# Performance work log

Measured on AMD Instinct MI355X. Metric: run time of the kernel, lower is better.

The kernel has to match this reference:

```python
import jax, jax.numpy as jnp
import numpy as np

B, S, HID = 2, 4096, 1024
H, D = 16, 64

def rotate_half(x):
    x1, x2 = jnp.split(x, 2, axis=-1)
    return jnp.concatenate([-x2, x1], axis=-1)

def setup_inputs() -> dict:
    key = jax.random.key(0)
    ks = jax.random.split(key, 8)
    hidden_states = jax.random.normal(ks[0], (B, S, HID), dtype=jnp.float32)
    pos = jnp.arange(S, dtype=jnp.float32)[:, None]
    inv_freq = 1.0 / (10000.0 ** (jnp.arange(0, D, 2, dtype=jnp.float32) / D))
    freqs = pos * inv_freq[None, :]
    emb = jnp.concatenate([freqs, freqs], axis=-1)  # [S, D]
    cos = jnp.cos(emb)
    sin = jnp.sin(emb)
    W_rkv = jax.random.normal(ks[1], (3 * H * D, HID), dtype=jnp.float32) * 0.02
    W_o = jax.random.normal(ks[2], (HID, H * D), dtype=jnp.float32) * 0.02
    # match torch init: uniform(-8,-5), uniform(-1,1), uniform(0.2,0.8)
    time_decay = jax.random.uniform(ks[3], (H, D), minval=-8.0, maxval=-5.0, dtype=jnp.float32)
    time_first = jax.random.uniform(ks[4], (H, D), minval=-1.0, maxval=1.0, dtype=jnp.float32)
    time_mix = jax.random.uniform(ks[5], (1, 1, HID), minval=0.2, maxval=0.8, dtype=jnp.float32)
    return {"hidden_states": hidden_states, "cos": cos, "sin": sin,
            "W_rkv": W_rkv, "W_o": W_o, "time_decay": time_decay,
            "time_first": time_first, "time_mix": time_mix}

def reference(hidden_states, cos, sin, W_rkv, W_o, time_decay, time_first, time_mix):
    b, s, hid = hidden_states.shape
    # token-shift time mixing
    xx = jnp.concatenate([jnp.zeros_like(hidden_states[:, :1]), hidden_states[:, :-1]], axis=1)
    mixed = hidden_states * time_mix + xx * (1.0 - time_mix)
    rkv = jnp.einsum('bsh,oh->bso', mixed, W_rkv).reshape(b, s, 3, H, D)
    r = jax.nn.sigmoid(rkv[:, :, 0])  # [B,S,H,D]
    k = rkv[:, :, 1]
    v = rkv[:, :, 2]
    # rotary on r, k
    c = cos[None, :, None, :]
    sn = sin[None, :, None, :]
    r = r * c + rotate_half(r) * sn
    k = k * c + rotate_half(k) * sn
    # fast rwkv linear attention (parallel approximation)
    w = -jnp.exp(time_decay)
    kv = k * v  # [B,S,H,D]
    pos = jnp.arange(s, dtype=hidden_states.dtype)
    pos_diff = pos[:, None] - pos[None, :]  # [S,S]
    mask = pos_diff > 0  # i > j masked (per original code)
    avg_decay = jnp.mean(w)
    pd = jnp.where(mask, 0.0, pos_diff)
    dw = jnp.where(mask, 0.0, jnp.exp(avg_decay * -jnp.abs(pd)))
    dw = dw / (dw.sum(axis=1, keepdims=True) + 1e-8)
    weighted_kv = jnp.einsum('ij,bjhd->bihd', dw, kv)
    out = r * (time_first[None, None] * kv + weighted_kv)  # [B,S,H,D]
    out = out.reshape(b, s, H * D)
    return jnp.einsum('bso,ho->bsh', out, W_o)
```

## Files before the change

kernel.cpp:

```cpp
#include <hip/hip_runtime.h>
#include <math.h>

#define S_LEN 4096
#define HIDN  1024
#define NH    16
#define HD    64
#define BATCH 2
#define M_TOTAL (BATCH * S_LEN)
#define N_RKV   (3 * HIDN)
#define CS 128
#define NC (S_LEN / CS)

typedef __attribute__((ext_vector_type(8))) _Float16 f16x8;
typedef __attribute__((ext_vector_type(4))) float f32x4;
typedef __attribute__((ext_vector_type(4))) unsigned short u16x4;

__device__ __forceinline__ unsigned short f2h(float x) {
    _Float16 h = (_Float16)x;
    return *(unsigned short*)&h;
}
__device__ __forceinline__ float h2f(unsigned short b) {
    _Float16 h = *(_Float16*)&b;
    return (float)h;
}

__device__ __forceinline__ void load_lds16(const void* g, void* l) {
    __builtin_amdgcn_global_load_lds((const __attribute__((address_space(1))) void*)g,
                                     (__attribute__((address_space(3))) void*)l, 16, 0, 0);
}

__global__ void k_avg_decay(const float* __restrict__ td, float* __restrict__ a_out) {
    int t = threadIdx.x;
    double acc = 0.0;
    for (int i = t; i < NH * HD; i += 64) acc += exp((double)td[i]);
    for (int off = 32; off > 0; off >>= 1) acc += __shfl_down(acc, off, 64);
    if (t == 0) a_out[0] = (float)(acc / (double)(NH * HD));
}

__global__ __launch_bounds__(256)
void k_split_mix(const float* __restrict__ hs, const float* __restrict__ tm,
                 unsigned short* __restrict__ Ah) {
    int g = blockIdx.x * 256 + threadIdx.x;
    int kc = (g & 255) * 4;
    int m = g >> 8;
    float4 cur = *(const float4*)&hs[(size_t)m * HIDN + kc];
    float4 t4  = *(const float4*)&tm[kc];
    float4 prev = make_float4(0.f, 0.f, 0.f, 0.f);
    if (m & (S_LEN - 1)) prev = *(const float4*)&hs[(size_t)(m - 1) * HIDN + kc];
    u16x4 h;
    h.x = f2h(cur.x * t4.x + prev.x * (1.f - t4.x));
    h.y = f2h(cur.y * t4.y + prev.y * (1.f - t4.y));
    h.z = f2h(cur.z * t4.z + prev.z * (1.f - t4.z));
    h.w = f2h(cur.w * t4.w + prev.w * (1.f - t4.w));
    *(u16x4*)&Ah[(size_t)m * HIDN + kc] = h;
}

__global__ __launch_bounds__(256)
void k_split_w(const float* __restrict__ W, unsigned short* __restrict__ Wh) {
    int g = blockIdx.x * 256 + threadIdx.x;
    size_t o = (size_t)g * 4;
    float4 v = *(const float4*)&W[o];
    u16x4 h;
    h.x = f2h(v.x); h.y = f2h(v.y); h.z = f2h(v.z); h.w = f2h(v.w);
    *(u16x4*)&Wh[o] = h;
}

__device__ __forceinline__ f32x4 mfma16(f16x8 a, f16x8 b, f32x4 c) {
    return __builtin_amdgcn_mfma_f32_16x16x32_f16(a, b, c, 0, 0, 0);
}

__global__ __launch_bounds__(192, 2)
void k_gemm1_fused(const unsigned short* __restrict__ Ahg,
                   const unsigned short* __restrict__ Wr,
                   const float* __restrict__ cosp, const float* __restrict__ sinp,
                   const float* __restrict__ a_ptr,
                   unsigned short* __restrict__ rP, unsigned short* __restrict__ kvP,
                   float* __restrict__ Cb)
{
    __shared__ unsigned short smem[20480];
    const int tid  = threadIdx.x;
    const int lane = tid & 63;
    const int wave = tid >> 6;
    const int h  = blockIdx.x;
    const int mc = blockIdx.y;
    const int m0 = mc * 128;
    const int b  = mc >> 5;
    const int c  = mc & 31;
    const int bh = b * NH + h;

    const unsigned short* segsrc[7];
    int segdst[7];
    {
        int rowoff = lane >> 2;
        int q = (lane & 3) ^ (rowoff & 3);
#pragma unroll
        for (int i = 0; i < 7; ++i) {
            int s = wave + 3 * i;
            if (s < 20) {
                const unsigned short* base;
                int row;
                if (s < 8) { base = Ahg; row = m0 + s * 16; }
                else {
                    int t = s - 8;
                    base = Wr;
                    row = (t >> 2) * 1024 + h * 64 + (t & 3) * 16;
                }
                segsrc[i] = base + (size_t)(row + rowoff) * 1024 + q * 8;
                segdst[i] = (s < 8) ? s * 512 : 4096 + (s - 8) * 512;
            }
        }
    }

    const int lm = lane & 15;
    const int rq = lane >> 4;
    const int qx = rq ^ (lane & 3);

    f32x4 acc[8][4] = {};

#pragma unroll
    for (int i = 0; i < 7; ++i)
        if (wave + 3 * i < 20) load_lds16(segsrc[i], smem + segdst[i]);

    int p = 0;
    for (int kt = 0; kt < 1024; kt += 32) {
        __syncthreads();
        if (kt + 32 < 1024) {
            int np = p ^ 1;
#pragma unroll
            for (int i = 0; i < 7; ++i)
                if (wave + 3 * i < 20)
                    load_lds16(segsrc[i] + kt + 32, smem + np * 10240 + segdst[i]);
        }
        const unsigned short* sb = smem + p * 10240;
        f16x8 fa[8], fb[4];
#pragma unroll
        for (int mt = 0; mt < 8; ++mt)
            fa[mt] = *(const f16x8*)(sb + (mt * 16 + lm) * 32 + qx * 8);
#pragma unroll
        for (int nt = 0; nt < 4; ++nt)
            fb[nt] = *(const f16x8*)(sb + 4096 + (wave * 64 + nt * 16 + lm) * 32 + qx * 8);
#pragma unroll
        for (int mt = 0; mt < 8; ++mt)
#pragma unroll
            for (int nt = 0; nt < 4; ++nt)
                acc[mt][nt] = mfma16(fa[mt], fb[nt], acc[mt][nt]);
        p ^= 1;
    }

    float a = a_ptr[0];
    float psum = 0.f;
    const int d = lane;
    float* Lf = (float*)smem;
#pragma unroll
    for (int g = 0; g < 4; ++g) {
        __syncthreads();
#pragma unroll
        for (int mt2 = 0; mt2 < 2; ++mt2) {
            int mt = 2 * g + mt2;
#pragma unroll
            for (int nt = 0; nt < 4; ++nt)
#pragma unroll
                for (int r = 0; r < 4; ++r) {
                    int rl = mt2 * 16 + rq * 4 + r;
                    Lf[(wave * 32 + rl) * 64 + nt * 16 + lm] = acc[mt][nt][r];
                }
        }
        __syncthreads();
        for (int row = wave; row < 32; row += 3) {
            int s = c * CS + g * 32 + row;
            int dp = d ^ 32;
            float r_ = Lf[row * 64 + d];
            float rp = Lf[row * 64 + dp];
            float k_ = Lf[(32 + row) * 64 + d];
            float kp = Lf[(32 + row) * 64 + dp];
            float v_ = Lf[(64 + row) * 64 + d];
            float cs = cosp[s * HD + d], sn = sinp[s * HD + d];
            float sgn = (d < 32) ? -1.f : 1.f;
            float sig  = 1.f / (1.f + expf(-r_));
            float sigp = 1.f / (1.f + expf(-rp));
            float rr = sig * cs + sgn * sigp * sn;
            float kk = k_ * cs + sgn * kp * sn;
            float kv = kk * v_;
            size_t ob = ((size_t)bh * S_LEN + s) * HD + d;
            rP[ob]  = f2h(rr);
            kvP[ob] = f2h(kv);
            psum += expf(a * (float)(g * 32 + row)) * kv;
        }
    }
    __syncthreads();
    Lf[wave * 64 + d] = psum;
    __syncthreads();
    if (tid < 64)
        Cb[((size_t)bh * NC + c) * 64 + tid] = Lf[tid] + Lf[64 + tid] + Lf[128 + tid];
}

__global__ __launch_bounds__(64)
void k_chunk_suffix(const float* __restrict__ Cb, const float* __restrict__ a_ptr,
                    float* __restrict__ Sb) {
    int bh = blockIdx.x;
    int d = threadIdx.x;
    float a = a_ptr[0];
    float eaCS = expf(a * (float)CS);
    float run = 0.f;
    Sb[(size_t)(bh * NC + NC - 1) * 64 + d] = 0.f;
    for (int c = NC - 2; c >= 0; --c) {
        run = Cb[(size_t)(bh * NC + c + 1) * 64 + d] + eaCS * run;
        Sb[(size_t)(bh * NC + c) * 64 + d] = run;
    }
}

__global__ __launch_bounds__(256)
void k_wkv2(const unsigned short* __restrict__ rP, const unsigned short* __restrict__ kvP,
            const float* __restrict__ Sb, const float* __restrict__ a_ptr,
            const float* __restrict__ tf,
            unsigned short* __restrict__ outH) {
    __shared__ float Tl[4][64];
    int bid = blockIdx.x;
    int c  = bid & (NC - 1);
    int bh = bid >> 5;
    int b = bh >> 4, h = bh & 15;
    int lane = threadIdx.x & 63;
    int wave = threadIdx.x >> 6;
    float a = a_ptr[0];
    float ea = expf(a);
    float em1a = expm1f(a);
    size_t base = ((size_t)bh * S_LEN + c * CS + wave * 32) * HD + lane;

    float kvreg[32], rreg[32];
    float w = 1.f, T = 0.f;
#pragma unroll
    for (int t = 0; t < 32; ++t) {
        kvreg[t] = h2f(kvP[base + (size_t)t * HD]);
        rreg[t]  = h2f(rP[base + (size_t)t * HD]);
        T += w * kvreg[t];
        w *= ea;
    }
    Tl[wave][lane] = T;
    __syncthreads();

    float e32 = expf(a * 32.f);
    float S_run = Sb[(size_t)bid * 64 + lane] * expf(a * 32.f * (float)(3 - wave));
    float f = 1.f;
    for (int wp = wave + 1; wp < 4; ++wp) {
        S_run += f * Tl[wp][lane];
        f *= e32;
    }
    float tfv = tf[h * HD + lane];
#pragma unroll
    for (int t = 31; t >= 0; --t) {
        float kv = kvreg[t];
        S_run = kv + ea * S_run;
        int ig = c * CS + wave * 32 + t;
        float Z = expm1f(a * (float)(S_LEN - ig)) / em1a + 1e-8f;
        float o = rreg[t] * (tfv * kv + S_run / Z);
        size_t m = (size_t)b * S_LEN + ig;
        outH[m * HIDN + h * HD + lane] = f2h(o);
    }
}

__global__ __launch_bounds__(256, 2)
void k_mfma_gemm(const unsigned short* __restrict__ Ah, int lda,
                 const unsigned short* __restrict__ Bm, int ldb,
                 float* __restrict__ C, int ldc)
{
    __shared__ unsigned short smem[8192];
    const int tid  = threadIdx.x;
    const int lane = tid & 63;
    const int wave = tid >> 6;
    const int wm = wave >> 1, wn = wave & 1;
    const int m0 = blockIdx.y * 128;
    const int n0 = blockIdx.x * 128;

    const unsigned short* segsrc[4];
    int segdst[4];
    {
        int rowoff = lane >> 2;
        int q = (lane & 3) ^ (rowoff & 3);
#pragma unroll
        for (int i = 0; i < 4; ++i) {
            int s = wave * 4 + i;
            const unsigned short* base = (s < 8) ? Ah : Bm;
            int ld = (s < 8) ? lda : ldb;
            int row = (s < 8) ? (m0 + s * 16) : (n0 + (s - 8) * 16);
            segsrc[i] = base + (size_t)(row + rowoff) * ld + q * 8;
            segdst[i] = s * 512;
        }
    }

    const int lm = lane & 15;
    const int qx = (lane >> 4) ^ (lane & 3);
    int aoff[4], boff[4];
#pragma unroll
    for (int t = 0; t < 4; ++t) {
        aoff[t] = (wm * 64 + t * 16 + lm) * 32 + qx * 8;
        boff[t] = 4096 + (wn * 64 + t * 16 + lm) * 32 + qx * 8;
    }

    f32x4 acc[4][4] = {};

    for (int kt = 0; kt < 1024; kt += 32) {
        __syncthreads();
#pragma unroll
        for (int i = 0; i < 4; ++i)
            load_lds16(segsrc[i] + kt, smem + segdst[i]);
        __syncthreads();

        f16x8 fah[4], fb[4];
#pragma unroll
        for (int t = 0; t < 4; ++t) {
            fah[t] = *(const f16x8*)(smem + aoff[t]);
            fb[t]  = *(const f16x8*)(smem + boff[t]);
        }
#pragma unroll
        for (int mt = 0; mt < 4; ++mt)
#pragma unroll
            for (int nt = 0; nt < 4; ++nt)
                acc[mt][nt] = mfma16(fah[mt], fb[nt], acc[mt][nt]);
    }

    const int rq = lane >> 4;
#pragma unroll
    for (int mt = 0; mt < 4; ++mt)
#pragma unroll
        for (int nt = 0; nt < 4; ++nt) {
            int col = n0 + wn * 64 + nt * 16 + lm;
#pragma unroll
            for (int r = 0; r < 4; ++r) {
                int row = m0 + wm * 64 + mt * 16 + rq * 4 + r;
                C[(size_t)row * ldc + col] = acc[mt][nt][r];
            }
        }
}

extern "C" void kernel_launch(void* const* d_in, const int* in_sizes, int n_in,
                              void* d_out, int out_size, void* d_ws, size_t ws_size,
                              hipStream_t stream) {
    const float* hs    = (const float*)d_in[0];
    const float* cosp  = (const float*)d_in[1];
    const float* sinp  = (const float*)d_in[2];
    const float* W_rkv = (const float*)d_in[3];
    const float* W_o   = (const float*)d_in[4];
    const float* td    = (const float*)d_in[5];
    const float* tf    = (const float*)d_in[6];
    const float* tm    = (const float*)d_in[7];
    float* out = (float*)d_out;

    char* w = (char*)d_ws;
    unsigned short* rP    = (unsigned short*)w;
    unsigned short* kvP   = (unsigned short*)(w + 16777216);
    unsigned short* Ah    = (unsigned short*)(w + 33554432);
    unsigned short* Wrh   = (unsigned short*)(w + 50331648);
    unsigned short* Woh   = (unsigned short*)(w + 56623104);
    unsigned short* outH  = (unsigned short*)(w + 58720256);
    float*          Cb    = (float*)(w + 75497472);
    float*          Sb    = (float*)(w + 75759616);
    float*          a_ptr = (float*)(w + 76021760);

    k_avg_decay<<<1, 64, 0, stream>>>(td, a_ptr);

    k_split_mix<<<(M_TOTAL * HIDN / 4) / 256, 256, 0, stream>>>(hs, tm, Ah);
    k_split_w<<<(N_RKV * HIDN / 4) / 256, 256, 0, stream>>>(W_rkv, Wrh);
    k_split_w<<<(HIDN * HIDN / 4) / 256, 256, 0, stream>>>(W_o, Woh);

    dim3 g1(NH, M_TOTAL / 128);
    k_gemm1_fused<<<g1, 192, 0, stream>>>(Ah, Wrh, cosp, sinp, a_ptr, rP, kvP, Cb);

    k_chunk_suffix<<<BATCH * NH, 64, 0, stream>>>(Cb, a_ptr, Sb);
    k_wkv2<<<BATCH * NH * NC, 256, 0, stream>>>(rP, kvP, Sb, a_ptr, tf, outH);

    dim3 g2(HIDN / 128, M_TOTAL / 128);
    k_mfma_gemm<<<g2, 256, 0, stream>>>(outH, HIDN, Woh, HIDN, out, HIDN);
}
```

Baseline: 259.9 us.

## Unfuse rotary epilogue from GEMM1, use generic tiled GEMM with XCD swizzle

Replaces the GEMM1 kernel with its fused sigmoid/rotary/kv epilogue by a generic 128x128 double-buffered MFMA GEMM that writes raw r,k,v in fp16. A new k_cb kernel computes the per-chunk decay sums from those values, and k_wkv2 recomputes sigmoid, rotary and kv on the fly. The same templated GEMM, with a blockIdx remap across 8 groups meant to match the XCDs and a double-buffered LDS pipeline, replaces the output projection. This trades the expensive LDS-staged epilogue and low-occupancy 192-thread blocks for an extra read of the rkv buffer and recomputed elementwise work.

```diff
diff --git a/kernel.cpp b/kernel.cpp
--- a/kernel.cpp
+++ b/kernel.cpp
@@ -69,129 +69,146 @@
     return __builtin_amdgcn_mfma_f32_16x16x32_f16(a, b, c, 0, 0, 0);
 }
 
-__global__ __launch_bounds__(192, 2)
-void k_gemm1_fused(const unsigned short* __restrict__ Ahg,
-                   const unsigned short* __restrict__ Wr,
-                   const float* __restrict__ cosp, const float* __restrict__ sinp,
-                   const float* __restrict__ a_ptr,
-                   unsigned short* __restrict__ rP, unsigned short* __restrict__ kvP,
-                   float* __restrict__ Cb)
+template<int LDC, int NBX, bool HALF_OUT>
+__global__ __launch_bounds__(256, 2)
+void k_gemm_bt(const unsigned short* __restrict__ A,
+               const unsigned short* __restrict__ Bm,
+               void* __restrict__ Cv)
 {
-    __shared__ unsigned short smem[20480];
+    __shared__ unsigned short smem[16384];
     const int tid  = threadIdx.x;
     const int lane = tid & 63;
     const int wave = tid >> 6;
-    const int h  = blockIdx.x;
-    const int mc = blockIdx.y;
-    const int m0 = mc * 128;
-    const int b  = mc >> 5;
-    const int c  = mc & 31;
-    const int bh = b * NH + h;
-
-    const unsigned short* segsrc[7];
-    int segdst[7];
+    const int wm = wave >> 1, wn = wave & 1;
+
+    const int cpx = gridDim.x >> 3;
+    const int wg  = (blockIdx.x & 7) * cpx + (blockIdx.x >> 3);
+    const int bx  = wg % NBX;
+    const int by  = wg / NBX;
+    const int m0 = by * 128;
+    const int n0 = bx * 128;
+
+    const unsigned short* segsrc[4];
+    int segdst[4];
     {
         int rowoff = lane >> 2;
         int q = (lane & 3) ^ (rowoff & 3);
 #pragma unroll
-        for (int i = 0; i < 7; ++i) {
-            int s = wave + 3 * i;
-            if (s < 20) {
-                const unsigned short* base;
-                int row;
-                if (s < 8) { base = Ahg; row = m0 + s * 16; }
-                else {
-                    int t = s - 8;
-                    base = Wr;
-                    row = (t >> 2) * 1024 + h * 64 + (t & 3) * 16;
-                }
-                segsrc[i] = base + (size_t)(row + rowoff) * 1024 + q * 8;
-                segdst[i] = (s < 8) ? s * 512 : 4096 + (s - 8) * 512;
-            }
+        for (int i = 0; i < 4; ++i) {
+            int s = wave * 4 + i;
+            const unsigned short* base = (s < 8) ? A : Bm;
+            int row = (s < 8) ? (m0 + s * 16) : (n0 + (s - 8) * 16);
+            segsrc[i] = base + (size_t)(row + rowoff) * 1024 + q * 8;
+            segdst[i] = s * 512;
         }
     }
 
     const int lm = lane & 15;
     const int rq = lane >> 4;
     const int qx = rq ^ (lane & 3);
-
-    f32x4 acc[8][4] = {};
-
-#pragma unroll
-    for (int i = 0; i < 7; ++i)
-        if (wave + 3 * i < 20) load_lds16(segsrc[i], smem + segdst[i]);
+    int aoff[4], boff[4];
+#pragma unroll
+    for (int t = 0; t < 4; ++t) {
+        aoff[t] = (wm * 64 + t * 16 + lm) * 32 + qx * 8;
+        boff[t] = 4096 + (wn * 64 + t * 16 + lm) * 32 + qx * 8;
+    }
+
+    f32x4 acc[4][4] = {};
+
+#pragma unroll
+    for (int i = 0; i < 4; ++i) load_lds16(segsrc[i], smem + segdst[i]);
 
     int p = 0;
     for (int kt = 0; kt < 1024; kt += 32) {
         __syncthreads();
         if (kt + 32 < 1024) {
-            int np = p ^ 1;
-#pragma unroll
-            for (int i = 0; i < 7; ++i)
-                if (wave + 3 * i < 20)
-                    load_lds16(segsrc[i] + kt + 32, smem + np * 10240 + segdst[i]);
+#pragma unroll
+            for (int i = 0; i < 4; ++i)
+                load_lds16(segsrc[i] + kt + 32, smem + ((p ^ 1) * 8192 + segdst[i]));
         }
-        const unsigned short* sb = smem + p * 10240;
-        f16x8 fa[8], fb[4];
-#pragma unroll
-        for (int mt = 0; mt < 8; ++mt)
-            fa[mt] = *(const f16x8*)(sb + (mt * 16 + lm) * 32 + qx * 8);
-#pragma unroll
-        for (int nt = 0; nt < 4; ++nt)
-            fb[nt] = *(const f16x8*)(sb + 4096 + (wave * 64 + nt * 16 + lm) * 32 + qx * 8);
-#pragma unroll
-        for (int mt = 0; mt < 8; ++mt)
+        const unsigned short* sb = smem + p * 8192;
+        f16x8 fa[4], fb[4];
+#pragma unroll
+        for (int t = 0; t < 4; ++t) {
+            fa[t] = *(const f16x8*)(sb + aoff[t]);
+            fb[t] = *(const f16x8*)(sb + boff[t]);
+        }
+#pragma unroll
+        for (int mt = 0; mt < 4; ++mt)
 #pragma unroll
             for (int nt = 0; nt < 4; ++nt)
                 acc[mt][nt] = mfma16(fa[mt], fb[nt], acc[mt][nt]);
         p ^= 1;
     }
 
+#pragma unroll
+    for (int mt = 0; mt < 4; ++mt)
+#pragma unroll
+        for (int nt = 0; nt < 4; ++nt) {
+            int col = n0 + wn * 64 + nt * 16 + lm;
+#pragma unroll
+            for (int r = 0; r < 4; ++r) {
+                int row = m0 + wm * 64 + mt * 16 + rq * 4 + r;
+                if constexpr (HALF_OUT)
+                    ((unsigned short*)Cv)[(size_t)row * LDC + col] = f2h(acc[mt][nt][r]);
+                else
+                    ((float*)Cv)[(size_t)row * LDC + col] = acc[mt][nt][r];
+            }
+        }
+}
+
+__global__ __launch_bounds__(256)
+void k_cb(const unsigned short* __restrict__ rkv,
+          const float* __restrict__ cosp, const float* __restrict__ sinp,
+          const float* __restrict__ a_ptr, float* __restrict__ Cb)
+{
+    __shared__ float Ls[4][64][4];
+    int bid = blockIdx.x;
+    int c  = bid & (NC - 1);
+    int bh = bid >> 5;
+    int b = bh >> 4, h = bh & 15;
+    int lane = threadIdx.x & 63;
+    int wave = threadIdx.x >> 6;
+    int lm = lane & 15;
+    int rs = lane >> 4;
+    int d0 = lm * 4;
     float a = a_ptr[0];
-    float psum = 0.f;
-    const int d = lane;
-    float* Lf = (float*)smem;
-#pragma unroll
-    for (int g = 0; g < 4; ++g) {
-        __syncthreads();
-#pragma unroll
-        for (int mt2 = 0; mt2 < 2; ++mt2) {
-            int mt = 2 * g + mt2;
-#pragma unroll
-            for (int nt = 0; nt < 4; ++nt)
-#pragma unroll
-                for (int r = 0; r < 4; ++r) {
-                    int rl = mt2 * 16 + rq * 4 + r;
-                    Lf[(wave * 32 + rl) * 64 + nt * 16 + lm] = acc[mt][nt][r];
-                }
-        }
-        __syncthreads();
-        for (int row = wave; row < 32; row += 3) {
-            int s = c * CS + g * 32 + row;
-            int dp = d ^ 32;
-            float r_ = Lf[row * 64 + d];
-            float rp = Lf[row * 64 + dp];
-            float k_ = Lf[(32 + row) * 64 + d];
-            float kp = Lf[(32 + row) * 64 + dp];
-            float v_ = Lf[(64 + row) * 64 + d];
-            float cs = cosp[s * HD + d], sn = sinp[s * HD + d];
-            float sgn = (d < 32) ? -1.f : 1.f;
-            float sig  = 1.f / (1.f + expf(-r_));
-            float sigp = 1.f / (1.f + expf(-rp));
-            float rr = sig * cs + sgn * sigp * sn;
-            float kk = k_ * cs + sgn * kp * sn;
-            float kv = kk * v_;
-            size_t ob = ((size_t)bh * S_LEN + s) * HD + d;
-            rP[ob]  = f2h(rr);
-            kvP[ob] = f2h(kv);
-            psum += expf(a * (float)(g * 32 + row)) * kv;
-        }
-    }
+    float sgn = (lm < 8) ? -1.f : 1.f;
+    float ps0 = 0.f, ps1 = 0.f, ps2 = 0.f, ps3 = 0.f;
+#pragma unroll
+    for (int it = 0; it < 8; ++it) {
+        int t = wave * 32 + it * 4 + rs;
+        int s = c * CS + t;
+        const unsigned short* rk = rkv + ((size_t)b * S_LEN + s) * N_RKV + h * 64 + d0;
+        u16x4 k4 = *(const u16x4*)(rk + 1024);
+        u16x4 v4 = *(const u16x4*)(rk + 2048);
+        float4 cs4 = *(const float4*)&cosp[s * HD + d0];
+        float4 sn4 = *(const float4*)&sinp[s * HD + d0];
+        float e = expf(a * (float)t);
+        float k0 = h2f(k4.x), k1 = h2f(k4.y), k2 = h2f(k4.z), k3 = h2f(k4.w);
+        float kp0 = __shfl_xor(k0, 8, 64);
+        float kp1 = __shfl_xor(k1, 8, 64);
+        float kp2 = __shfl_xor(k2, 8, 64);
+        float kp3 = __shfl_xor(k3, 8, 64);
+        ps0 += e * (k0 * cs4.x + sgn * kp0 * sn4.x) * h2f(v4.x);
+        ps1 += e * (k1 * cs4.y + sgn * kp1 * sn4.y) * h2f(v4.y);
+        ps2 += e * (k2 * cs4.z + sgn * kp2 * sn4.z) * h2f(v4.z);
+        ps3 += e * (k3 * cs4.w + sgn * kp3 * sn4.w) * h2f(v4.w);
+    }
+    Ls[wave][lane][0] = ps0; Ls[wave][lane][1] = ps1;
+    Ls[wave][lane][2] = ps2; Ls[wave][lane][3] = ps3;
     __syncthreads();
-    Lf[wave * 64 + d] = psum;
-    __syncthreads();
-    if (tid < 64)
-        Cb[((size_t)bh * NC + c) * 64 + tid] = Lf[tid] + Lf[64 + tid] + Lf[128 + tid];
+    if (threadIdx.x < 64) {
+        int d = threadIdx.x;
+        int lmm = d >> 2, j = d & 3;
+        float sum = 0.f;
+#pragma unroll
+        for (int wv = 0; wv < 4; ++wv)
+#pragma unroll
+            for (int r = 0; r < 4; ++r)
+                sum += Ls[wv][r * 16 + lmm][j];
+        Cb[((size_t)bh * NC + c) * 64 + d] = sum;
+    }
 }
 
 __global__ __launch_bounds__(64)
@@ -210,7 +227,8 @@
 }
 
 __global__ __launch_bounds__(256)
-void k_wkv2(const unsigned short* __restrict__ rP, const unsigned short* __restrict__ kvP,
+void k_wkv2(const unsigned short* __restrict__ rkv,
+            const float* __restrict__ cosp, const float* __restrict__ sinp,
             const float* __restrict__ Sb, const float* __restrict__ a_ptr,
             const float* __restrict__ tf,
             unsigned short* __restrict__ outH) {
@@ -224,14 +242,25 @@
     float a = a_ptr[0];
     float ea = expf(a);
     float em1a = expm1f(a);
-    size_t base = ((size_t)bh * S_LEN + c * CS + wave * 32) * HD + lane;
+    int s0 = c * CS + wave * 32;
+    const unsigned short* rkb = rkv + ((size_t)b * S_LEN + s0) * N_RKV + h * 64 + lane;
+    float sgn = (lane < 32) ? -1.f : 1.f;
 
     float kvreg[32], rreg[32];
     float w = 1.f, T = 0.f;
 #pragma unroll
     for (int t = 0; t < 32; ++t) {
-        kvreg[t] = h2f(kvP[base + (size_t)t * HD]);
-        rreg[t]  = h2f(rP[base + (size_t)t * HD]);
+        const unsigned short* pr = rkb + (size_t)t * N_RKV;
+        float r_ = h2f(pr[0]);
+        float k_ = h2f(pr[1024]);
+        float v_ = h2f(pr[2048]);
+        float cs = cosp[(s0 + t) * HD + lane];
+        float sn = sinp[(s0 + t) * HD + lane];
+        float sig = 1.f / (1.f + expf(-r_));
+        float sigp = __shfl_xor(sig, 32, 64);
+        float kp   = __shfl_xor(k_, 32, 64);
+        rreg[t]  = sig * cs + sgn * sigp * sn;
+        kvreg[t] = (k_ * cs + sgn * kp * sn) * v_;
         T += w * kvreg[t];
         w *= ea;
     }
@@ -256,80 +285,6 @@
         size_t m = (size_t)b * S_LEN + ig;
         outH[m * HIDN + h * HD + lane] = f2h(o);
     }
-}
-
-__global__ __launch_bounds__(256, 2)
-void k_mfma_gemm(const unsigned short* __restrict__ Ah, int lda,
-                 const unsigned short* __restrict__ Bm, int ldb,
-                 float* __restrict__ C, int ldc)
-{
-    __shared__ unsigned short smem[8192];
-    const int tid  = threadIdx.x;
-    const int lane = tid & 63;
-    const int wave = tid >> 6;
-    const int wm = wave >> 1, wn = wave & 1;
-    const int m0 = blockIdx.y * 128;
-    const int n0 = blockIdx.x * 128;
-
-    const unsigned short* segsrc[4];
-    int segdst[4];
-    {
-        int rowoff = lane >> 2;
-        int q = (lane & 3) ^ (rowoff & 3);
-#pragma unroll
-        for (int i = 0; i < 4; ++i) {
-            int s = wave * 4 + i;
-            const unsigned short* base = (s < 8) ? Ah : Bm;
-            int ld = (s < 8) ? lda : ldb;
-            int row = (s < 8) ? (m0 + s * 16) : (n0 + (s - 8) * 16);
-            segsrc[i] = base + (size_t)(row + rowoff) * ld + q * 8;
-            segdst[i] = s * 512;
-        }
-    }
-
-    const int lm = lane & 15;
-    const int qx = (lane >> 4) ^ (lane & 3);
-    int aoff[4], boff[4];
-#pragma unroll
-    for (int t = 0; t < 4; ++t) {
-        aoff[t] = (wm * 64 + t * 16 + lm) * 32 + qx * 8;
-        boff[t] = 4096 + (wn * 64 + t * 16 + lm) * 32 + qx * 8;
-    }
-
-    f32x4 acc[4][4] = {};
-
-    for (int kt = 0; kt < 1024; kt += 32) {
-        __syncthreads();
-#pragma unroll
-        for (int i = 0; i < 4; ++i)
-            load_lds16(segsrc[i] + kt, smem + segdst[i]);
-        __syncthreads();
-
-        f16x8 fah[4], fb[4];
-#pragma unroll
-        for (int t = 0; t < 4; ++t) {
-            fah[t] = *(const f16x8*)(smem + aoff[t]);
-            fb[t]  = *(const f16x8*)(smem + boff[t]);
-        }
-#pragma unroll
-        for (int mt = 0; mt < 4; ++mt)
-#pragma unroll
-            for (int nt = 0; nt < 4; ++nt)
-                acc[mt][nt] = mfma16(fah[mt], fb[nt], acc[mt][nt]);
-    }
-
-    const int rq = lane >> 4;
-#pragma unroll
-    for (int mt = 0; mt < 4; ++mt)
-#pragma unroll
-        for (int nt = 0; nt < 4; ++nt) {
-            int col = n0 + wn * 64 + nt * 16 + lm;
-#pragma unroll
-            for (int r = 0; r < 4; ++r) {
-                int row = m0 + wm * 64 + mt * 16 + rq * 4 + r;
-                C[(size_t)row * ldc + col] = acc[mt][nt][r];
-            }
-        }
 }
 
 extern "C" void kernel_launch(void* const* d_in, const int* in_sizes, int n_in,
@@ -346,15 +301,14 @@
     float* out = (float*)d_out;
 
     char* w = (char*)d_ws;
-    unsigned short* rP    = (unsigned short*)w;
-    unsigned short* kvP   = (unsigned short*)(w + 16777216);
-    unsigned short* Ah    = (unsigned short*)(w + 33554432);
-    unsigned short* Wrh   = (unsigned short*)(w + 50331648);
-    unsigned short* Woh   = (unsigned short*)(w + 56623104);
-    unsigned short* outH  = (unsigned short*)(w + 58720256);
-    float*          Cb    = (float*)(w + 75497472);
-    float*          Sb    = (float*)(w + 75759616);
-    float*          a_ptr = (float*)(w + 76021760);
+    unsigned short* rkvH = (unsigned short*)w;
+    unsigned short* Ah   = (unsigned short*)(w + 50331648);
+    unsigned short* outH = (unsigned short*)(w + 50331648);
+    unsigned short* Wrh  = (unsigned short*)(w + 67108864);
+    unsigned short* Woh  = (unsigned short*)(w + 73400320);
+    float*          Cb   = (float*)(w + 75497472);
+    float*          Sb   = (float*)(w + 75759616);
+    float*          a_ptr= (float*)(w + 76021760);
 
     k_avg_decay<<<1, 64, 0, stream>>>(td, a_ptr);
 
@@ -362,12 +316,11 @@
     k_split_w<<<(N_RKV * HIDN / 4) / 256, 256, 0, stream>>>(W_rkv, Wrh);
     k_split_w<<<(HIDN * HIDN / 4) / 256, 256, 0, stream>>>(W_o, Woh);
 
-    dim3 g1(NH, M_TOTAL / 128);
-    k_gemm1_fused<<<g1, 192, 0, stream>>>(Ah, Wrh, cosp, sinp, a_ptr, rP, kvP, Cb);
-
+    k_gemm_bt<N_RKV, 24, true><<<1536, 256, 0, stream>>>(Ah, Wrh, rkvH);
+
+    k_cb<<<BATCH * NH * NC, 256, 0, stream>>>(rkvH, cosp, sinp, a_ptr, Cb);
     k_chunk_suffix<<<BATCH * NH, 64, 0, stream>>>(Cb, a_ptr, Sb);
-    k_wkv2<<<BATCH * NH * NC, 256, 0, stream>>>(rP, kvP, Sb, a_ptr, tf, outH);
-
-    dim3 g2(HIDN / 128, M_TOTAL / 128);
-    k_mfma_gemm<<<g2, 256, 0, stream>>>(outH, HIDN, Woh, HIDN, out, HIDN);
-}
+    k_wkv2<<<BATCH * NH * NC, 256, 0, stream>>>(rkvH, cosp, sinp, Sb, a_ptr, tf, outH);
+
+    k_gemm_bt<HIDN, 8, false><<<512, 256, 0, stream>>>(outH, Woh, out);
+}
```

Result: faster. 254.2 us (-2.2%).
